# Kernel tuning notes

Measured on AMD Instinct MI355X. Metric: run time of the kernel, lower is better.

The kernel has to match this reference:

```python
import jax, jax.numpy as jnp
import numpy as np

N_NODES = 50000
N_EDGES = 600000
N_GRAPHS = 256
N_FL1, N_MPL, N_FL2, N_FL3 = 128, 128, 128, 64
EPS = 1e-12


def _glorot(key, shape):
    lim = float(np.sqrt(6.0 / (shape[0] + shape[1])))
    return jax.random.uniform(key, shape, jnp.float32, -lim, lim)


def setup_inputs() -> dict:
    key = jax.random.key(0)
    ks = jax.random.split(key, 16)
    x = jax.random.normal(ks[0], (N_NODES, 5), jnp.float32)
    edge_index = jax.random.randint(ks[1], (2, N_EDGES), 0, N_NODES, jnp.int64)
    batch = jnp.sort(jax.random.randint(ks[2], (N_NODES,), 0, N_GRAPHS, jnp.int64))
    return {
        "x": x,
        "edge_index": edge_index,
        "batch": batch,
        "W_pre": _glorot(ks[3], (5, N_FL1)),
        "b_pre": jnp.zeros((N_FL1,), jnp.float32),
        "W1_l": _glorot(ks[4], (N_FL1, N_MPL)),
        "b1": jnp.zeros((N_MPL,), jnp.float32),
        "W1_r": _glorot(ks[5], (N_FL1, N_MPL)),
        "W2_l": _glorot(ks[6], (N_MPL, N_MPL)),
        "b2": jnp.zeros((N_MPL,), jnp.float32),
        "W2_r": _glorot(ks[7], (N_MPL, N_MPL)),
        "W_p1": _glorot(ks[8], (N_MPL, N_FL2)),
        "b_p1": jnp.zeros((N_FL2,), jnp.float32),
        "W_p2": _glorot(ks[9], (N_FL2, N_FL3)),
        "b_p2": jnp.zeros((N_FL3,), jnp.float32),
        "W_out": _glorot(ks[10], (N_FL3, 1)),
        "b_out": jnp.zeros((1,), jnp.float32),
    }


def _sage_conv(x, src, dst, deg_inv, W_l, b_l, W_r):
    # mean-aggregate neighbor messages x[src] onto dst, then linear transforms
    agg = jax.ops.segment_sum(x[src], dst, num_segments=N_NODES) * deg_inv  # [N, d]
    out = agg @ W_l + b_l + x @ W_r
    # normalize=True -> L2 normalize per node (PyG F.normalize, eps=1e-12)
    norm = jnp.sqrt(jnp.sum(out * out, axis=-1, keepdims=True))
    return out / jnp.maximum(norm, EPS)


def reference(x, edge_index, batch, W_pre, b_pre, W1_l, b1, W1_r,
              W2_l, b2, W2_r, W_p1, b_p1, W_p2, b_p2, W_out, b_out):
    src, dst = edge_index[0], edge_index[1]
    deg = jax.ops.segment_sum(jnp.ones((N_EDGES,), jnp.float32), dst, num_segments=N_NODES)
    deg_inv = (1.0 / jnp.maximum(deg, 1.0))[:, None]

    h = jax.nn.relu(x @ W_pre + b_pre)
    h = jax.nn.relu(_sage_conv(h, src, dst, deg_inv, W1_l, b1, W1_r))
    h = jax.nn.relu(_sage_conv(h, src, dst, deg_inv, W2_l, b2, W2_r))

    # global_mean_pool over graph ids in batch
    g_sum = jax.ops.segment_sum(h, batch, num_segments=N_GRAPHS)  # [G, d]
    g_cnt = jax.ops.segment_sum(jnp.ones((N_NODES,), jnp.float32), batch, num_segments=N_GRAPHS)
    g = g_sum / jnp.maximum(g_cnt, 1.0)[:, None]

    g = jax.nn.relu(g @ W_p1 + b_p1)
    g = jax.nn.relu(g @ W_p2 + b_p2)
    return g @ W_out + b_out  # [G, 1]
```

## Files before the change

kernel.cpp:

```cpp
#include <hip/hip_runtime.h>
#include <hip/hip_bf16.h>

#define N_NODES 50000
#define N_EDGES 600000
#define N_GRAPHS 256
#define D 128
#define NTILES 1563

typedef __bf16 bf16x8 __attribute__((ext_vector_type(8)));
typedef float f32x16 __attribute__((ext_vector_type(16)));
typedef unsigned short u16x8 __attribute__((ext_vector_type(8)));
typedef unsigned short u16x4 __attribute__((ext_vector_type(4)));

__device__ __forceinline__ float bf2f(unsigned short u) {
    unsigned v = ((unsigned)u) << 16;
    return __builtin_bit_cast(float, v);
}
__device__ __forceinline__ unsigned short f2bf(float f) {
    unsigned x = __builtin_bit_cast(unsigned, f);
    unsigned r = (x + 0x7fffu + ((x >> 16) & 1u)) >> 16;
    return (unsigned short)r;
}


#define ZERO_N (50048 + 32768)
#define ZERO_BLOCKS 324
#define PACK_BLOCKS 256
#define PRE_BLOCKS 3125

__global__ __launch_bounds__(256) void init_kernel(
    int* __restrict__ deg_gsum,
    const float* __restrict__ Wl1, const float* __restrict__ Wr1,
    const float* __restrict__ Wl2, const float* __restrict__ Wr2,
    unsigned short* __restrict__ Wpk,
    const float* __restrict__ x, const float* __restrict__ Wpre,
    const float* __restrict__ bpre, unsigned short* __restrict__ h0) {
    int bb = blockIdx.x;
    if (bb < ZERO_BLOCKS) {
        int i = bb * 256 + threadIdx.x;
        if (i < ZERO_N) deg_gsum[i] = 0;
    } else if (bb < ZERO_BLOCKS + PACK_BLOCKS) {
        int tid = (bb - ZERO_BLOCKS) * 256 + threadIdx.x;
        int conv = tid >> 15;
        int e = tid & 32767;
        int j = e & 7, lane = (e >> 3) & 63, ct = (e >> 9) & 3, kt = e >> 11;
        int k = kt * 16 + (lane >> 5) * 8 + j;
        int col = (lane & 31) * 4 + ct;
        const float* Wl = conv ? Wl2 : Wl1;
        const float* Wr = conv ? Wr2 : Wr1;
        float v = (k < 128) ? Wl[k * 128 + col] : Wr[(k - 128) * 128 + col];
        Wpk[tid] = f2bf(v);
    } else {
        int idx = (bb - ZERO_BLOCKS - PACK_BLOCKS) * 256 + threadIdx.x;
        if (idx >= N_NODES * 16) return;
        int node = idx >> 4, j8 = (idx & 15) * 8;
        const float* xr = x + node * 5;
        float acc[8];
#pragma unroll
        for (int c = 0; c < 8; ++c) acc[c] = bpre[j8 + c];
#pragma unroll
        for (int k = 0; k < 5; ++k) {
            float xv = xr[k];
#pragma unroll
            for (int c = 0; c < 8; ++c) acc[c] += xv * Wpre[k * D + j8 + c];
        }
        u16x8 o;
#pragma unroll
        for (int c = 0; c < 8; ++c) o[c] = f2bf(fmaxf(acc[c], 0.f));
        *(u16x8*)&h0[(size_t)node * D + j8] = o;
    }
}


__global__ void deg_kernel(const int* __restrict__ dst, int* __restrict__ deg) {
    int e = blockIdx.x * 256 + threadIdx.x;
    if (e < N_EDGES) atomicAdd(&deg[dst[e]], 1);
}

__global__ __launch_bounds__(1024) void scan_blk_kernel(const int* __restrict__ deg,
                                                        int* __restrict__ partial,
                                                        int* __restrict__ bsum) {
    __shared__ int tmp[1024];
    int tid = threadIdx.x;
    int i = blockIdx.x * 1024 + tid;
    int v = (i < N_NODES) ? deg[i] : 0;
    tmp[tid] = v;
    __syncthreads();
    for (int off = 1; off < 1024; off <<= 1) {
        int add = (tid >= off) ? tmp[tid - off] : 0;
        __syncthreads();
        tmp[tid] += add;
        __syncthreads();
    }
    if (i < N_NODES) partial[i] = tmp[tid] - v;
    if (tid == 1023) bsum[blockIdx.x] = tmp[tid];
}

__global__ __launch_bounds__(256) void scan_fix_kernel(const int* __restrict__ partial,
                                                       const int* __restrict__ bsum,
                                                       const int* __restrict__ deg,
                                                       int* __restrict__ row_start,
                                                       int* __restrict__ cursor,
                                                       float* __restrict__ deg_inv) {
    __shared__ int boff_s;
    int bucket = (blockIdx.x * 256) >> 10;
    if (threadIdx.x < 64) {
        int l = threadIdx.x;
        int v = (l < bucket) ? bsum[l] : 0;
#pragma unroll
        for (int m = 32; m >= 1; m >>= 1) v += __shfl_xor(v, m);
        if (l == 0) boff_s = v;
    }
    __syncthreads();
    int i = blockIdx.x * 256 + threadIdx.x;
    if (i >= N_NODES) return;
    int dg = deg[i];
    int rs = partial[i] + boff_s;
    row_start[i] = rs;
    cursor[i] = rs;
    deg_inv[i] = 1.0f / fmaxf((float)dg, 1.0f);
    if (i == N_NODES - 1) row_start[N_NODES] = rs + dg;
}

__global__ void fill_kernel(const int* __restrict__ src, const int* __restrict__ dst,
                            int* __restrict__ cursor, int* __restrict__ csr_src) {
    int e = blockIdx.x * 256 + threadIdx.x;
    if (e < N_EDGES) {
        int slot = atomicAdd(&cursor[dst[e]], 1);
        csr_src[slot] = src[e];
    }
}


__global__ __launch_bounds__(256) void agg_kernel(const unsigned short* __restrict__ h,
                                                  const int* __restrict__ row_start,
                                                  const int* __restrict__ csr_src,
                                                  const float* __restrict__ deg_inv,
                                                  unsigned short* __restrict__ aggb) {
    int node = blockIdx.x * 16 + (threadIdx.x >> 4);
    int fl = threadIdx.x & 15;
    if (node >= N_NODES) return;
    int s = row_start[node], e = row_start[node + 1];
    float a[8] = {0.f, 0.f, 0.f, 0.f, 0.f, 0.f, 0.f, 0.f};
    int i = s;
    for (; i + 7 < e; i += 8) {
        int c[8];
#pragma unroll
        for (int q = 0; q < 8; ++q) c[q] = csr_src[i + q];
        bf16x8 v[8];
#pragma unroll
        for (int q = 0; q < 8; ++q) v[q] = *(const bf16x8*)(h + (size_t)c[q] * D + fl * 8);
#pragma unroll
        for (int q = 0; q < 8; ++q)
#pragma unroll
            for (int j = 0; j < 8; ++j) a[j] += (float)v[q][j];
    }
    for (; i + 3 < e; i += 4) {
        int c[4];
#pragma unroll
        for (int q = 0; q < 4; ++q) c[q] = csr_src[i + q];
        bf16x8 v[4];
#pragma unroll
        for (int q = 0; q < 4; ++q) v[q] = *(const bf16x8*)(h + (size_t)c[q] * D + fl * 8);
#pragma unroll
        for (int q = 0; q < 4; ++q)
#pragma unroll
            for (int j = 0; j < 8; ++j) a[j] += (float)v[q][j];
    }
    for (; i < e; ++i) {
        int c0 = csr_src[i];
        bf16x8 v0 = *(const bf16x8*)(h + (size_t)c0 * D + fl * 8);
#pragma unroll
        for (int j = 0; j < 8; ++j) a[j] += (float)v0[j];
    }
    float di = deg_inv[node];
    u16x8 o;
#pragma unroll
    for (int j = 0; j < 8; ++j) o[j] = f2bf(a[j] * di);
    *(u16x8*)(aggb + (size_t)node * D + fl * 8) = o;
}


__global__ __launch_bounds__(64) void lin_mfma_kernel(const unsigned short* __restrict__ hin,
                                                      const unsigned short* __restrict__ aggb,
                                                      const unsigned short* __restrict__ Wp,
                                                      const float* __restrict__ b,
                                                      unsigned short* __restrict__ hout) {
    int wg = blockIdx.x;
    int lane = threadIdx.x;
    int l31 = lane & 31, hi = lane >> 5;
    int row0 = wg * 32;
    int rowg = row0 + l31;
    if (rowg > N_NODES - 1) rowg = N_NODES - 1;

    const unsigned short* arow = aggb + (size_t)rowg * D + hi * 8;
    const unsigned short* hrow = hin + (size_t)rowg * D + hi * 8;
    const unsigned short* wbase = Wp + lane * 8;

    f32x16 acc[4];
#pragma unroll
    for (int ct = 0; ct < 4; ++ct) acc[ct] = (f32x16)(0.0f);

#pragma unroll
    for (int kt = 0; kt < 16; ++kt) {
        const unsigned short* asrc = (kt < 8) ? (arow + kt * 16) : (hrow + (kt - 8) * 16);
        bf16x8 af = *(const bf16x8*)asrc;
#pragma unroll
        for (int ct = 0; ct < 4; ++ct) {
            bf16x8 bfrag = *(const bf16x8*)(wbase + (kt * 4 + ct) * 512);
            acc[ct] = __builtin_amdgcn_mfma_f32_32x32x16_bf16(af, bfrag, acc[ct], 0, 0, 0);
        }
    }

    float4 b4 = *(const float4*)&b[l31 * 4];
    float bb[4] = {b4.x, b4.y, b4.z, b4.w};

#pragma unroll
    for (int r = 0; r < 16; ++r) {
        float v[4];
        float ss = 0.f;
#pragma unroll
        for (int ct = 0; ct < 4; ++ct) {
            v[ct] = acc[ct][r] + bb[ct];
            ss += v[ct] * v[ct];
        }
        ss += __shfl_xor(ss, 1);
        ss += __shfl_xor(ss, 2);
        ss += __shfl_xor(ss, 4);
        ss += __shfl_xor(ss, 8);
        ss += __shfl_xor(ss, 16);
        float sc = 1.0f / fmaxf(sqrtf(ss), 1e-12f);
        int row = row0 + (r & 3) + 8 * (r >> 2) + 4 * hi;
        if (row < N_NODES) {
            u16x4 o;
#pragma unroll
            for (int ct = 0; ct < 4; ++ct) o[ct] = f2bf(fmaxf(v[ct] * sc, 0.f));
            *(u16x4*)(hout + (size_t)row * D + l31 * 4) = o;
        }
    }
}


__global__ __launch_bounds__(128) void pool_sum_kernel(const unsigned short* __restrict__ h,
                                                       const int* __restrict__ batch,
                                                       float* __restrict__ gsum) {
    int j = threadIdx.x;
    int i0 = blockIdx.x * 128;
    int i1 = i0 + 128;
    if (i1 > N_NODES) i1 = N_NODES;
    __shared__ int bids[128];
    if (i0 + j < N_NODES) bids[j] = batch[i0 + j];
    __syncthreads();
    float acc = 0.f;
    int cur = bids[0];
    for (int i = i0; i < i1; ++i) {
        int bid = bids[i - i0];
        if (bid != cur) {
            atomicAdd(&gsum[cur * D + j], acc);
            acc = 0.f;
            cur = bid;
        }
        acc += bf2f(h[(size_t)i * D + j]);
    }
    atomicAdd(&gsum[cur * D + j], acc);
}


__global__ __launch_bounds__(128) void mlp_kernel(const float* __restrict__ gsum,
                                                  const int* __restrict__ batch,
                                                  const float* __restrict__ Wp1,
                                                  const float* __restrict__ bp1,
                                                  const float* __restrict__ Wp2,
                                                  const float* __restrict__ bp2,
                                                  const float* __restrict__ Wout,
                                                  const float* __restrict__ bout,
                                                  float* __restrict__ out) {
    __shared__ float gin[128], y1[128], y2[64];
    __shared__ float cnt_s;
    int gid = blockIdx.x, j = threadIdx.x;
    if (j == 0) {
        int lo = 0, hi = N_NODES;
        while (lo < hi) { int m = (lo + hi) >> 1; if (batch[m] < gid) lo = m + 1; else hi = m; }
        int start = lo;
        lo = start; hi = N_NODES;
        while (lo < hi) { int m = (lo + hi) >> 1; if (batch[m] < gid + 1) lo = m + 1; else hi = m; }
        cnt_s = fmaxf((float)(lo - start), 1.0f);
    }
    __syncthreads();
    gin[j] = gsum[gid * 128 + j] / cnt_s;
    __syncthreads();
    float a = bp1[j];
    for (int k = 0; k < 128; ++k) a += gin[k] * Wp1[k * 128 + j];
    y1[j] = fmaxf(a, 0.f);
    __syncthreads();
    if (j < 64) {
        float a2 = bp2[j];
        for (int k = 0; k < 128; ++k) a2 += y1[k] * Wp2[k * 64 + j];
        y2[j] = fmaxf(a2, 0.f);
    }
    __syncthreads();
    if (j < 64) {
        float v = y2[j] * Wout[j];
#pragma unroll
        for (int m = 32; m >= 1; m >>= 1) v += __shfl_xor(v, m);
        if (j == 0) out[gid] = v + bout[0];
    }
}


extern "C" void kernel_launch(void* const* d_in, const int* in_sizes, int n_in,
                              void* d_out, int out_size, void* d_ws, size_t ws_size,
                              hipStream_t stream) {
    const float* x     = (const float*)d_in[0];
    const int*   ei    = (const int*)d_in[1];
    const int*   batch = (const int*)d_in[2];
    const float* W_pre = (const float*)d_in[3];
    const float* b_pre = (const float*)d_in[4];
    const float* W1_l  = (const float*)d_in[5];
    const float* b1    = (const float*)d_in[6];
    const float* W1_r  = (const float*)d_in[7];
    const float* W2_l  = (const float*)d_in[8];
    const float* b2    = (const float*)d_in[9];
    const float* W2_r  = (const float*)d_in[10];
    const float* W_p1  = (const float*)d_in[11];
    const float* b_p1  = (const float*)d_in[12];
    const float* W_p2  = (const float*)d_in[13];
    const float* b_p2  = (const float*)d_in[14];
    const float* W_out = (const float*)d_in[15];
    const float* b_out = (const float*)d_in[16];

    const int* src = ei;
    const int* dst = ei + N_EDGES;

    size_t off = 0;
    auto carve = [&](size_t bytes) {
        void* p = (char*)d_ws + off;
        off += (bytes + 255) & ~(size_t)255;
        return p;
    };
    int* deg       = (int*)carve(50048 * 4 + 32768 * 4);
    float* gsum    = (float*)(deg + 50048);
    int* row_start = (int*)carve((N_NODES + 1) * 4);
    int* cursor    = (int*)carve(N_NODES * 4);
    int* csr_src   = (int*)carve(N_EDGES * 4);
    float* deg_inv = (float*)carve(N_NODES * 4);
    int* partial   = (int*)carve(N_NODES * 4);
    int* bsum      = (int*)carve(64 * 4);
    unsigned short* h0   = (unsigned short*)carve((size_t)N_NODES * D * 2);
    unsigned short* h1   = (unsigned short*)carve((size_t)N_NODES * D * 2);
    unsigned short* aggb = (unsigned short*)carve((size_t)N_NODES * D * 2);
    unsigned short* Wp   = (unsigned short*)carve(65536 * 2);
    unsigned short* h2 = h0;
    float* out = (float*)d_out;

    const int nblk_scan = (N_NODES + 1023) / 1024;

    init_kernel<<<ZERO_BLOCKS + PACK_BLOCKS + PRE_BLOCKS, 256, 0, stream>>>(
        deg, W1_l, W1_r, W2_l, W2_r, Wp, x, W_pre, b_pre, h0);

    deg_kernel<<<(N_EDGES + 255) / 256, 256, 0, stream>>>(dst, deg);
    scan_blk_kernel<<<nblk_scan, 1024, 0, stream>>>(deg, partial, bsum);
    scan_fix_kernel<<<(N_NODES + 255) / 256, 256, 0, stream>>>(partial, bsum, deg,
                                                               row_start, cursor, deg_inv);
    fill_kernel<<<(N_EDGES + 255) / 256, 256, 0, stream>>>(src, dst, cursor, csr_src);

    agg_kernel<<<(N_NODES + 15) / 16, 256, 0, stream>>>(h0, row_start, csr_src, deg_inv, aggb);
    lin_mfma_kernel<<<NTILES, 64, 0, stream>>>(h0, aggb, Wp, b1, h1);

    agg_kernel<<<(N_NODES + 15) / 16, 256, 0, stream>>>(h1, row_start, csr_src, deg_inv, aggb);
    lin_mfma_kernel<<<NTILES, 64, 0, stream>>>(h1, aggb, Wp + 32768, b2, h2);

    pool_sum_kernel<<<(N_NODES + 127) / 128, 128, 0, stream>>>(h2, batch, gsum);
    mlp_kernel<<<N_GRAPHS, 128, 0, stream>>>(gsum, batch, W_p1, b_p1, W_p2, b_p2,
                                             W_out, b_out, out);
}
```

Measured before the change: 212.9 us.

## Stage packed weights in LDS shared by four waves per block in linear MFMA kernel

The linear MFMA kernel now runs four 32-row tiles per 256-thread block and copies the 64 KB packed weight matrix into shared memory once per block, instead of every wave reading it from global/L2. Each wave also prefetches all 16 A fragments into registers before the MFMA loop. This is meant to cut redundant weight traffic and hide activation load latency. The cost is 64 KB of LDS per block, which limits occupancy, plus more registers for the prefetched fragments.

```diff
diff --git a/kernel.cpp b/kernel.cpp
--- a/kernel.cpp
+++ b/kernel.cpp
@@ -181,21 +181,40 @@
 }
 
 
-__global__ __launch_bounds__(64) void lin_mfma_kernel(const unsigned short* __restrict__ hin,
-                                                      const unsigned short* __restrict__ aggb,
-                                                      const unsigned short* __restrict__ Wp,
-                                                      const float* __restrict__ b,
-                                                      unsigned short* __restrict__ hout) {
-    int wg = blockIdx.x;
-    int lane = threadIdx.x;
+__global__ __launch_bounds__(256) void lin_mfma_kernel(const unsigned short* __restrict__ hin,
+                                                       const unsigned short* __restrict__ aggb,
+                                                       const unsigned short* __restrict__ Wp,
+                                                       const float* __restrict__ b,
+                                                       unsigned short* __restrict__ hout) {
+    __shared__ unsigned short Wls[32768];
+
+    int t = threadIdx.x;
+    int wg = blockIdx.x * 4 + (t >> 6);
+    int lane = t & 63;
     int l31 = lane & 31, hi = lane >> 5;
     int row0 = wg * 32;
     int rowg = row0 + l31;
-    if (rowg > N_NODES - 1) rowg = N_NODES - 1;
-
-    const unsigned short* arow = aggb + (size_t)rowg * D + hi * 8;
-    const unsigned short* hrow = hin + (size_t)rowg * D + hi * 8;
-    const unsigned short* wbase = Wp + lane * 8;
+    bool wvalid = wg < NTILES;
+    int rowc = (wvalid && rowg < N_NODES) ? rowg : (N_NODES - 1);
+
+    const unsigned short* arow = aggb + (size_t)rowc * D + hi * 8;
+    const unsigned short* hrow = hin + (size_t)rowc * D + hi * 8;
+    bf16x8 afr[16];
+#pragma unroll
+    for (int kt = 0; kt < 8; ++kt) afr[kt] = *(const bf16x8*)(arow + kt * 16);
+#pragma unroll
+    for (int kt = 0; kt < 8; ++kt) afr[8 + kt] = *(const bf16x8*)(hrow + kt * 16);
+
+#pragma unroll
+    for (int q = 0; q < 16; ++q) {
+        int idx = q * 256 + t;
+        *(u16x8*)&Wls[idx * 8] = *(const u16x8*)&Wp[idx * 8];
+    }
+    __syncthreads();
+
+    if (!wvalid) return;
+
+    const unsigned short* wbase = Wls + lane * 8;
 
     f32x16 acc[4];
 #pragma unroll
@@ -203,12 +222,10 @@
 
 #pragma unroll
     for (int kt = 0; kt < 16; ++kt) {
-        const unsigned short* asrc = (kt < 8) ? (arow + kt * 16) : (hrow + (kt - 8) * 16);
-        bf16x8 af = *(const bf16x8*)asrc;
 #pragma unroll
         for (int ct = 0; ct < 4; ++ct) {
             bf16x8 bfrag = *(const bf16x8*)(wbase + (kt * 4 + ct) * 512);
-            acc[ct] = __builtin_amdgcn_mfma_f32_32x32x16_bf16(af, bfrag, acc[ct], 0, 0, 0);
+            acc[ct] = __builtin_amdgcn_mfma_f32_32x32x16_bf16(afr[kt], bfrag, acc[ct], 0, 0, 0);
         }
     }
 
@@ -365,10 +382,10 @@
     fill_kernel<<<(N_EDGES + 255) / 256, 256, 0, stream>>>(src, dst, cursor, csr_src);
 
     agg_kernel<<<(N_NODES + 15) / 16, 256, 0, stream>>>(h0, row_start, csr_src, deg_inv, aggb);
-    lin_mfma_kernel<<<NTILES, 64, 0, stream>>>(h0, aggb, Wp, b1, h1);
+    lin_mfma_kernel<<<(NTILES + 3) / 4, 256, 0, stream>>>(h0, aggb, Wp, b1, h1);
 
     agg_kernel<<<(N_NODES + 15) / 16, 256, 0, stream>>>(h1, row_start, csr_src, deg_inv, aggb);
-    lin_mfma_kernel<<<NTILES, 64, 0, stream>>>(h1, aggb, Wp + 32768, b2, h2);
+    lin_mfma_kernel<<<(NTILES + 3) / 4, 256, 0, stream>>>(h1, aggb, Wp + 32768, b2, h2);
 
     pool_sum_kernel<<<(N_NODES + 127) / 128, 128, 0, stream>>>(h2, batch, gsum);
     mlp_kernel<<<N_GRAPHS, 128, 0, stream>>>(gsum, batch, W_p1, b_p1, W_p2, b_p2,
```

Measured after the change: 204.2 us. 4.1% less time.
